# Performance work log

Measured on AMD Instinct MI355X. Metric: run time of the kernel, lower is better.

The kernel has to match this reference:

```python
import jax, jax.numpy as jnp
import numpy as np
import math

IN_C = 512
OUT_C = 512
K = 3
STYLE = 512
EPS = 1e-8
MOD_SCALE = 1.0 / math.sqrt(STYLE)        # EqualLinear scale (lr_mul=1)
CONV_SCALE = 1.0 / math.sqrt(IN_C * K * K)  # ModulatedConv2d scale


def setup_inputs() -> dict:
    key = jax.random.key(0)
    k1, k2, k3, k4 = jax.random.split(key, 4)
    return {
        "x": jax.random.normal(k1, (8, IN_C, 64, 64), dtype=jnp.float32),
        "style": jax.random.normal(k2, (8, STYLE), dtype=jnp.float32),
        "mod_weight": jax.random.normal(k3, (IN_C, STYLE), dtype=jnp.float32),
        "mod_bias": jnp.ones((IN_C,), dtype=jnp.float32),
        "weight": jax.random.normal(k4, (1, OUT_C, IN_C, K, K), dtype=jnp.float32),
    }


def _per_sample_conv(xi, wi):
    # xi: [in_c, H, W], wi: [out_c, in_c, K, K]
    out = jax.lax.conv_general_dilated(
        xi[None], wi, window_strides=(1, 1), padding="SAME",
        dimension_numbers=("NCHW", "OIHW", "NCHW"))
    return out[0]


def reference(x, style, mod_weight, mod_bias, weight):
    # EqualLinear modulation: s = style @ (W*scale)^T + bias  -> [B, in_c]
    s = style @ (mod_weight * MOD_SCALE).T + mod_bias
    # per-sample modulated weight: [B, out_c, in_c, K, K]
    w = CONV_SCALE * weight * s[:, None, :, None, None]
    demod = jax.lax.rsqrt(jnp.sum(w * w, axis=(2, 3, 4), keepdims=True) + EPS)
    w = w * demod
    # grouped conv (groups=batch) == vmap of per-sample conv
    out = jax.vmap(_per_sample_conv)(x, w)  # [B, out_c, H, W]
    return out
```

## Files before the change

### kernel.cpp

```cpp
#include <hip/hip_runtime.h>
#include <hip/hip_bf16.h>

typedef __attribute__((ext_vector_type(8))) short bf16x8;
typedef __attribute__((ext_vector_type(4))) float f32x4;
typedef unsigned int u32;

#define MOD_SCALE 0.04419417382415922f
#define CONV_SCALE 0.014731391274719742f

__device__ __forceinline__ unsigned short f2bf(float f) {
  union { float f; u32 u; } v; v.f = f;
  u32 r = v.u + 0x7fffu + ((v.u >> 16) & 1u);
  return (unsigned short)(r >> 16);
}

__device__ __forceinline__ void gload_lds16(const void* g, void* l) {
  __builtin_amdgcn_global_load_lds(
      (const __attribute__((address_space(1))) u32*)g,
      (__attribute__((address_space(3))) u32*)l, 16, 0, 0);
}

__global__ void k_prep(const float* __restrict__ wsrc, ushort* __restrict__ wb,
                       float* __restrict__ wsq, float* __restrict__ zerobuf,
                       const float* __restrict__ style, const float* __restrict__ mw,
                       const float* __restrict__ mb, float* __restrict__ s) {
  if (blockIdx.x < 1024) {
    int idx = blockIdx.x * 256 + threadIdx.x;
    if (blockIdx.x == 0 && threadIdx.x < 16) zerobuf[threadIdx.x] = 0.f;
    const float* wp = wsrc + (size_t)idx * 9;
    float sq = 0.f;
    #pragma unroll
    for (int tap = 0; tap < 9; ++tap) {
      float v = wp[tap];
      sq += v * v;
      wb[tap * 262144 + idx] = f2bf(v);
    }
    wsq[idx] = sq;
  } else {
    int idx = (blockIdx.x - 1024) * 256 + threadIdx.x;
    int b = idx >> 9, ic = idx & 511;
    const float4* wr = (const float4*)(mw + ic * 512);
    const float4* sr = (const float4*)(style + b * 512);
    float acc = 0.f;
    #pragma unroll 4
    for (int k = 0; k < 128; ++k) {
      float4 a = wr[k], c = sr[k];
      acc += a.x * c.x + a.y * c.y + a.z * c.z + a.w * c.w;
    }
    s[idx] = acc * MOD_SCALE + mb[ic];
  }
}

__global__ void k_demod(const float* __restrict__ wsq, const float* __restrict__ s,
                        float* __restrict__ dscale) {
  int idx = blockIdx.x * 256 + threadIdx.x;
  int b = idx >> 9, oc = idx & 511;
  const float4* wq = (const float4*)(wsq + oc * 512);
  const float4* sp = (const float4*)(s + b * 512);
  float acc = 0.f;
  #pragma unroll 4
  for (int k = 0; k < 128; ++k) {
    float4 a = wq[k], c = sp[k];
    acc += a.x * c.x * c.x + a.y * c.y * c.y + a.z * c.z * c.z + a.w * c.w * c.w;
  }
  dscale[idx] = CONV_SCALE * rsqrtf(CONV_SCALE * CONV_SCALE * acc + 1e-8f);
}

__global__ void k_xform(const float* __restrict__ x, const float* __restrict__ s,
                        ushort* __restrict__ xsb) {
  const int y = blockIdx.x, b = blockIdx.y, ich = blockIdx.z;
  const int t = threadIdx.x;
  __shared__ ushort T[64 * 264];
  const int px = t & 63, iq = t >> 6;
  const int icbase = ich * 256;
  #pragma unroll
  for (int i = 0; i < 8; ++i) {
    int ic8 = i * 4 + iq;
    int ic0 = icbase + ic8 * 8;
    union { ushort u[8]; uint4 v; } pk;
    #pragma unroll
    for (int j = 0; j < 8; ++j) {
      int ic = ic0 + j;
      float v = x[(b * 512 + ic) * 4096 + y * 64 + px] * s[b * 512 + ic];
      pk.u[j] = f2bf(v);
    }
    *(uint4*)&T[px * 264 + ic8 * 8] = pk.v;
  }
  __syncthreads();
  const int ch = t & 31;
  ushort* obase = xsb + ((b * 64 + y) * 64) * 512 + icbase + ch * 8;
  #pragma unroll
  for (int i = 0; i < 8; ++i) {
    int p = i * 8 + (t >> 5);
    uint4 v = *(const uint4*)&T[p * 264 + ch * 8];
    *(uint4*)(obase + p * 512) = v;
  }
}

#define BUFB 79104
__global__ __launch_bounds__(256, 1) void k_conv(
    const ushort* __restrict__ wb, const ushort* __restrict__ xsb,
    const float* __restrict__ dscale, const float* __restrict__ zerobuf,
    float* __restrict__ out) {
  const int yb = blockIdx.x, ocb = blockIdx.y, b = blockIdx.z;
  const int t = threadIdx.x;
  const int wv = t >> 6, l = t & 63;
  const int ln = l & 15, lq = l >> 4;
  const int y0 = yb * 8;

  extern __shared__ char smem[];
  float* dss = (float*)(smem + 2 * BUFB);

  if (t < 64) dss[t] = dscale[b * 512 + ocb * 64 + t];

  f32x4 acc[2][4][4];
  #pragma unroll
  for (int rr = 0; rr < 2; ++rr)
    #pragma unroll
    for (int m = 0; m < 4; ++m)
      #pragma unroll
      for (int n = 0; n < 4; ++n)
        acc[rr][m][n] = f32x4{0.f, 0.f, 0.f, 0.f};

  const int aslot = lq ^ ((ln >> 1) & 3);
  int bslot[3];
  #pragma unroll
  for (int dx = 0; dx < 3; ++dx) bslot[dx] = lq ^ (((ln + dx) >> 1) & 3);

  const int a_ocl = t >> 2;
  const int a_qs = (t & 3) ^ ((a_ocl >> 1) & 3);
  const char* srcA = (const char*)(wb + (ocb * 64 + a_ocl) * 512 + a_qs * 8);
  const int a_dstw = wv * 1024;

  const char* bsrc[11];
  int bdstc[11];
  #pragma unroll
  for (int i = 0; i < 11; ++i) {
    int cid = i * 256 + t;
    int r = cid / 264;
    int rem = cid - r * 264;
    int c = rem >> 2, q = rem & 3;
    int yy = y0 - 1 + r, xx = c - 1;
    int qs = q ^ ((c >> 1) & 3);
    int geo_ok = (cid < 2640) && ((unsigned)yy < 64u) && ((unsigned)xx < 64u);
    bsrc[i] = geo_ok ? (const char*)(xsb + ((b * 64 + yy) * 64 + xx) * 512 + qs * 8)
                     : (const char*)nullptr;
    bdstc[i] = (i * 256 + wv * 64) * 16;
  }

  auto STAGE = [&](int boff, int icB) {
    char* Ab = smem + boff;
    char* Bb = smem + boff + 36864;
    #pragma unroll
    for (int i = 0; i < 9; ++i)
      gload_lds16(srcA + i * 524288 + icB, Ab + i * 4096 + a_dstw);
    #pragma unroll
    for (int i = 0; i < 10; ++i) {
      const char* src = bsrc[i] ? bsrc[i] + icB : (const char*)zerobuf;
      gload_lds16(src, Bb + bdstc[i]);
    }
    if (t < 80) {
      const char* src = bsrc[10] ? bsrc[10] + icB : (const char*)zerobuf;
      gload_lds16(src, Bb + bdstc[10]);
    }
  };

  auto COMPUTE = [&](int boff) {
    const char* Ab = smem + boff;
    const char* Bb = smem + boff + 36864;
    #pragma unroll
    for (int dx = 0; dx < 3; ++dx) {
      bf16x8 bfr[4][4];
      #pragma unroll
      for (int r4 = 0; r4 < 4; ++r4)
        #pragma unroll
        for (int n = 0; n < 4; ++n)
          bfr[r4][n] = *(const bf16x8*)(Bb + ((wv * 2 + r4) * 66 + n * 16 + ln + dx) * 64 + bslot[dx] * 16);
      #pragma unroll
      for (int dy = 0; dy < 3; ++dy) {
        const int tap = dy * 3 + dx;
        bf16x8 af[4];
        #pragma unroll
        for (int m = 0; m < 4; ++m)
          af[m] = *(const bf16x8*)(Ab + tap * 4096 + (m * 16 + ln) * 64 + aslot * 16);
        #pragma unroll
        for (int rr = 0; rr < 2; ++rr)
          #pragma unroll
          for (int m = 0; m < 4; ++m)
            #pragma unroll
            for (int n = 0; n < 4; ++n)
              acc[rr][m][n] = __builtin_amdgcn_mfma_f32_16x16x32_bf16(af[m], bfr[dy + rr][n], acc[rr][m][n], 0, 0, 0);
      }
    }
  };

  STAGE(0, 0);
  __syncthreads();
  #pragma unroll 1
  for (int it = 0; it < 16; ++it) {
    if (it < 15) STAGE(((it + 1) & 1) * BUFB, (it + 1) * 64);
    COMPUTE((it & 1) * BUFB);
    __syncthreads();
  }

  #pragma unroll
  for (int rr = 0; rr < 2; ++rr) {
    const int y_row = y0 + wv * 2 + rr;
    #pragma unroll
    for (int m = 0; m < 4; ++m) {
      #pragma unroll
      for (int r4 = 0; r4 < 4; ++r4) {
        const int oc_l = m * 16 + lq * 4 + r4;
        const float sc = dss[oc_l];
        float* op = out + ((b * 512 + ocb * 64 + oc_l) * 4096 + y_row * 64);
        #pragma unroll
        for (int n = 0; n < 4; ++n)
          op[n * 16 + ln] = acc[rr][m][n][r4] * sc;
      }
    }
  }
}

extern "C" void kernel_launch(void* const* d_in, const int* in_sizes, int n_in,
                              void* d_out, int out_size, void* d_ws, size_t ws_size,
                              hipStream_t stream) {
  const float* x     = (const float*)d_in[0];
  const float* style = (const float*)d_in[1];
  const float* mw    = (const float*)d_in[2];
  const float* mb    = (const float*)d_in[3];
  const float* wsrc  = (const float*)d_in[4];
  float* out = (float*)d_out;

  char* ws = (char*)d_ws;
  float*  zerobuf = (float*)(ws + 0);
  float*  s       = (float*)(ws + 256);
  float*  dscale  = (float*)(ws + 16640);
  float*  wsq     = (float*)(ws + 33024);
  ushort* wb      = (ushort*)(ws + 1081600);
  ushort* xsb     = (ushort*)(ws + 5800192);

  hipFuncSetAttribute(reinterpret_cast<const void*>(k_conv),
                      hipFuncAttributeMaxDynamicSharedMemorySize, 2 * BUFB + 256);

  k_prep<<<dim3(1040), dim3(256), 0, stream>>>(wsrc, wb, wsq, zerobuf, style, mw, mb, s);
  k_demod<<<dim3(16), dim3(256), 0, stream>>>(wsq, s, dscale);
  k_xform<<<dim3(64, 8, 2), dim3(256), 0, stream>>>(x, s, xsb);
  k_conv<<<dim3(8, 8, 8), dim3(256), 2 * BUFB + 256, stream>>>(wb, xsb, dscale, zerobuf, out);
}
```

Before: 187.2 us.

## Switch conv to 32x32x16 MFMA with ic-blocked layouts and two blocks per CU

```diff
diff --git a/kernel.cpp b/kernel.cpp
--- a/kernel.cpp
+++ b/kernel.cpp
@@ -2,7 +2,7 @@
 #include <hip/hip_bf16.h>
 
 typedef __attribute__((ext_vector_type(8))) short bf16x8;
-typedef __attribute__((ext_vector_type(4))) float f32x4;
+typedef __attribute__((ext_vector_type(16))) float f32x16;
 typedef unsigned int u32;
 
 #define MOD_SCALE 0.04419417382415922f
@@ -26,6 +26,8 @@
                        const float* __restrict__ mb, float* __restrict__ s) {
   if (blockIdx.x < 1024) {
     int idx = blockIdx.x * 256 + threadIdx.x;
+    int oc = idx >> 9, ic = idx & 511;
+    int icb = ic >> 4, icr = ic & 15;
     if (blockIdx.x == 0 && threadIdx.x < 16) zerobuf[threadIdx.x] = 0.f;
     const float* wp = wsrc + (size_t)idx * 9;
     float sq = 0.f;
@@ -33,7 +35,7 @@
     for (int tap = 0; tap < 9; ++tap) {
       float v = wp[tap];
       sq += v * v;
-      wb[tap * 262144 + idx] = f2bf(v);
+      wb[((tap * 32 + icb) * 512 + oc) * 16 + icr] = f2bf(v);
     }
     wsq[idx] = sq;
   } else {
@@ -68,128 +70,118 @@
 
 __global__ void k_xform(const float* __restrict__ x, const float* __restrict__ s,
                         ushort* __restrict__ xsb) {
-  const int y = blockIdx.x, b = blockIdx.y, ich = blockIdx.z;
+  const int y = blockIdx.x, b = blockIdx.y;
   const int t = threadIdx.x;
-  __shared__ ushort T[64 * 264];
-  const int px = t & 63, iq = t >> 6;
-  const int icbase = ich * 256;
+  const int px = t & 63, icq = t >> 6;
   #pragma unroll
   for (int i = 0; i < 8; ++i) {
-    int ic8 = i * 4 + iq;
-    int ic0 = icbase + ic8 * 8;
-    union { ushort u[8]; uint4 v; } pk;
-    #pragma unroll
-    for (int j = 0; j < 8; ++j) {
-      int ic = ic0 + j;
+    int icb = i * 4 + icq;
+    union { ushort u[16]; uint4 v[2]; } pk;
+    #pragma unroll
+    for (int j = 0; j < 16; ++j) {
+      int ic = icb * 16 + j;
       float v = x[(b * 512 + ic) * 4096 + y * 64 + px] * s[b * 512 + ic];
       pk.u[j] = f2bf(v);
     }
-    *(uint4*)&T[px * 264 + ic8 * 8] = pk.v;
-  }
-  __syncthreads();
-  const int ch = t & 31;
-  ushort* obase = xsb + ((b * 64 + y) * 64) * 512 + icbase + ch * 8;
-  #pragma unroll
-  for (int i = 0; i < 8; ++i) {
-    int p = i * 8 + (t >> 5);
-    uint4 v = *(const uint4*)&T[p * 264 + ch * 8];
-    *(uint4*)(obase + p * 512) = v;
-  }
-}
-
-#define BUFB 79104
-__global__ __launch_bounds__(256, 1) void k_conv(
+    ushort* dst = xsb + ((size_t)((b * 64 + y) * 32 + icb) * 64 + px) * 16;
+    *(uint4*)dst = pk.v[0];
+    *(uint4*)(dst + 8) = pk.v[1];
+  }
+}
+
+#define ABYTES 18432
+#define BBYTES 21120
+#define BUFB   39552
+__global__ __launch_bounds__(256, 2) void k_conv(
     const ushort* __restrict__ wb, const ushort* __restrict__ xsb,
     const float* __restrict__ dscale, const float* __restrict__ zerobuf,
     float* __restrict__ out) {
   const int yb = blockIdx.x, ocb = blockIdx.y, b = blockIdx.z;
   const int t = threadIdx.x;
   const int wv = t >> 6, l = t & 63;
-  const int ln = l & 15, lq = l >> 4;
-  const int y0 = yb * 8;
+  const int lc = l & 31, lh = l >> 5;
+  const int y0 = yb * 8, oc0 = ocb * 64;
 
   extern __shared__ char smem[];
   float* dss = (float*)(smem + 2 * BUFB);
-
-  if (t < 64) dss[t] = dscale[b * 512 + ocb * 64 + t];
-
-  f32x4 acc[2][4][4];
+  if (t < 64) dss[t] = dscale[b * 512 + oc0 + t];
+
+  f32x16 acc[2][2][2];
   #pragma unroll
   for (int rr = 0; rr < 2; ++rr)
     #pragma unroll
-    for (int m = 0; m < 4; ++m)
-      #pragma unroll
-      for (int n = 0; n < 4; ++n)
-        acc[rr][m][n] = f32x4{0.f, 0.f, 0.f, 0.f};
-
-  const int aslot = lq ^ ((ln >> 1) & 3);
-  int bslot[3];
-  #pragma unroll
-  for (int dx = 0; dx < 3; ++dx) bslot[dx] = lq ^ (((ln + dx) >> 1) & 3);
-
-  const int a_ocl = t >> 2;
-  const int a_qs = (t & 3) ^ ((a_ocl >> 1) & 3);
-  const char* srcA = (const char*)(wb + (ocb * 64 + a_ocl) * 512 + a_qs * 8);
-  const int a_dstw = wv * 1024;
-
-  const char* bsrc[11];
-  int bdstc[11];
-  #pragma unroll
-  for (int i = 0; i < 11; ++i) {
+    for (int ocf = 0; ocf < 2; ++ocf)
+      #pragma unroll
+      for (int pxf = 0; pxf < 2; ++pxf)
+        #pragma unroll
+        for (int k = 0; k < 16; ++k)
+          acc[rr][ocf][pxf][k] = 0.f;
+
+  const char* asrc[5];
+  #pragma unroll
+  for (int i = 0; i < 5; ++i) {
     int cid = i * 256 + t;
-    int r = cid / 264;
-    int rem = cid - r * 264;
-    int c = rem >> 2, q = rem & 3;
-    int yy = y0 - 1 + r, xx = c - 1;
-    int qs = q ^ ((c >> 1) & 3);
-    int geo_ok = (cid < 2640) && ((unsigned)yy < 64u) && ((unsigned)xx < 64u);
-    bsrc[i] = geo_ok ? (const char*)(xsb + ((b * 64 + yy) * 64 + xx) * 512 + qs * 8)
-                     : (const char*)nullptr;
-    bdstc[i] = (i * 256 + wv * 64) * 16;
-  }
-
-  auto STAGE = [&](int boff, int icB) {
-    char* Ab = smem + boff;
-    char* Bb = smem + boff + 36864;
-    #pragma unroll
-    for (int i = 0; i < 9; ++i)
-      gload_lds16(srcA + i * 524288 + icB, Ab + i * 4096 + a_dstw);
-    #pragma unroll
-    for (int i = 0; i < 10; ++i) {
-      const char* src = bsrc[i] ? bsrc[i] + icB : (const char*)zerobuf;
-      gload_lds16(src, Bb + bdstc[i]);
-    }
-    if (t < 80) {
-      const char* src = bsrc[10] ? bsrc[10] + icB : (const char*)zerobuf;
-      gload_lds16(src, Bb + bdstc[10]);
-    }
+    int tap = cid >> 7, rem = cid & 127;
+    int oc_l = rem >> 1, h = rem & 1;
+    asrc[i] = (const char*)wb + (size_t)tap * 524288 + (oc0 + oc_l) * 32 + h * 16;
+  }
+  const char* bsrc[6];
+  int bstride[6];
+  #pragma unroll
+  for (int i = 0; i < 6; ++i) {
+    int cid = i * 256 + t;
+    int r = cid / 132, rem = cid - r * 132;
+    int yy = y0 - 1 + r;
+    bool interior = (rem >= 2) && (rem < 130) && ((unsigned)yy < 64u);
+    bsrc[i] = interior
+        ? (const char*)xsb + (size_t)(b * 64 + yy) * 65536 + (rem - 2) * 16
+        : (const char*)zerobuf;
+    bstride[i] = interior ? 2048 : 0;
+  }
+
+  auto STAGE = [&](int bo, int icb) {
+    char* Ab = smem + bo;
+    char* Bb = Ab + ABYTES;
+    const int aoff = icb * 16384;
+    #pragma unroll
+    for (int i = 0; i < 4; ++i)
+      gload_lds16(asrc[i] + aoff, Ab + i * 4096 + wv * 1024);
+    if (t < 128)
+      gload_lds16(asrc[4] + aoff, Ab + 16384 + wv * 1024);
+    #pragma unroll
+    for (int i = 0; i < 5; ++i)
+      gload_lds16(bsrc[i] + icb * bstride[i], Bb + i * 4096 + wv * 1024);
+    if (t < 40)
+      gload_lds16(bsrc[5] + icb * bstride[5], Bb + 20480);
   };
 
-  auto COMPUTE = [&](int boff) {
-    const char* Ab = smem + boff;
-    const char* Bb = smem + boff + 36864;
+  auto COMPUTE = [&](int bo) {
+    const char* Ab = smem + bo;
+    const char* Bb = Ab + ABYTES;
+    const int arow = lc * 32 + lh * 16;
     #pragma unroll
     for (int dx = 0; dx < 3; ++dx) {
-      bf16x8 bfr[4][4];
-      #pragma unroll
-      for (int r4 = 0; r4 < 4; ++r4)
-        #pragma unroll
-        for (int n = 0; n < 4; ++n)
-          bfr[r4][n] = *(const bf16x8*)(Bb + ((wv * 2 + r4) * 66 + n * 16 + ln + dx) * 64 + bslot[dx] * 16);
+      bf16x8 bfr[4][2];
+      #pragma unroll
+      for (int j = 0; j < 4; ++j)
+        #pragma unroll
+        for (int pxf = 0; pxf < 2; ++pxf)
+          bfr[j][pxf] = *(const bf16x8*)(Bb + (wv * 2 + j) * 2112 + (pxf * 32 + dx + lc) * 32 + lh * 16);
       #pragma unroll
       for (int dy = 0; dy < 3; ++dy) {
         const int tap = dy * 3 + dx;
-        bf16x8 af[4];
-        #pragma unroll
-        for (int m = 0; m < 4; ++m)
-          af[m] = *(const bf16x8*)(Ab + tap * 4096 + (m * 16 + ln) * 64 + aslot * 16);
+        bf16x8 af[2];
+        #pragma unroll
+        for (int ocf = 0; ocf < 2; ++ocf)
+          af[ocf] = *(const bf16x8*)(Ab + tap * 2048 + ocf * 1024 + arow);
         #pragma unroll
         for (int rr = 0; rr < 2; ++rr)
           #pragma unroll
-          for (int m = 0; m < 4; ++m)
+          for (int ocf = 0; ocf < 2; ++ocf)
             #pragma unroll
-            for (int n = 0; n < 4; ++n)
-              acc[rr][m][n] = __builtin_amdgcn_mfma_f32_16x16x32_bf16(af[m], bfr[dy + rr][n], acc[rr][m][n], 0, 0, 0);
+            for (int pxf = 0; pxf < 2; ++pxf)
+              acc[rr][ocf][pxf] = __builtin_amdgcn_mfma_f32_32x32x16_bf16(
+                  af[ocf], bfr[rr + dy][pxf], acc[rr][ocf][pxf], 0, 0, 0);
       }
     }
   };
@@ -197,8 +189,8 @@
   STAGE(0, 0);
   __syncthreads();
   #pragma unroll 1
-  for (int it = 0; it < 16; ++it) {
-    if (it < 15) STAGE(((it + 1) & 1) * BUFB, (it + 1) * 64);
+  for (int it = 0; it < 32; ++it) {
+    if (it < 31) STAGE(((it + 1) & 1) * BUFB, it + 1);
     COMPUTE((it & 1) * BUFB);
     __syncthreads();
   }
@@ -207,15 +199,15 @@
   for (int rr = 0; rr < 2; ++rr) {
     const int y_row = y0 + wv * 2 + rr;
     #pragma unroll
-    for (int m = 0; m < 4; ++m) {
-      #pragma unroll
-      for (int r4 = 0; r4 < 4; ++r4) {
-        const int oc_l = m * 16 + lq * 4 + r4;
-        const float sc = dss[oc_l];
-        float* op = out + ((b * 512 + ocb * 64 + oc_l) * 4096 + y_row * 64);
-        #pragma unroll
-        for (int n = 0; n < 4; ++n)
-          op[n * 16 + ln] = acc[rr][m][n][r4] * sc;
+    for (int ocf = 0; ocf < 2; ++ocf) {
+      #pragma unroll
+      for (int pxf = 0; pxf < 2; ++pxf) {
+        #pragma unroll
+        for (int reg = 0; reg < 16; ++reg) {
+          int oc_l = ocf * 32 + (reg & 3) + 8 * (reg >> 2) + 4 * lh;
+          out[(size_t)(b * 512 + oc0 + oc_l) * 4096 + y_row * 64 + pxf * 32 + lc]
+              = acc[rr][ocf][pxf][reg] * dss[oc_l];
+        }
       }
     }
   }
@@ -244,6 +236,6 @@
 
   k_prep<<<dim3(1040), dim3(256), 0, stream>>>(wsrc, wb, wsq, zerobuf, style, mw, mb, s);
   k_demod<<<dim3(16), dim3(256), 0, stream>>>(wsq, s, dscale);
-  k_xform<<<dim3(64, 8, 2), dim3(256), 0, stream>>>(x, s, xsb);
+  k_xform<<<dim3(64, 8), dim3(256), 0, stream>>>(x, s, xsb);
   k_conv<<<dim3(8, 8, 8), dim3(256), 2 * BUFB + 256, stream>>>(wb, xsb, dscale, zerobuf, out);
 }
```

Result: no change. 185.6 us (-0.9%).
